# Kernel optimization log

Measured on AMD Instinct MI355X. Metric: run time of the kernel, lower is better.

Reference implementation:

```python
import jax, jax.numpy as jnp
import numpy as np

FOV_UP = 3.0 * np.pi / 180.0
FOV_DOWN = -25.0 * np.pi / 180.0
BIG = 1e9  # penalty to exclude invalid points from nearest-neighbor search


def rv_to_points(rv):
    """Spherical back-projection of a range image [H,W] -> xyz [H,W,3]."""
    H, W = rv.shape
    fov = FOV_UP - FOV_DOWN
    pitch = (1.0 - (jnp.arange(H, dtype=rv.dtype) + 0.5) / H) * fov + FOV_DOWN  # [H]
    yaw = -((jnp.arange(W, dtype=rv.dtype) + 0.5) / W * 2.0 - 1.0) * jnp.pi     # [W]
    cp = jnp.cos(pitch)[:, None]
    sp = jnp.sin(pitch)[:, None]
    x = rv * cp * jnp.cos(yaw)[None, :]
    y = rv * cp * jnp.sin(yaw)[None, :]
    z = rv * sp
    return jnp.stack([x, y, z], axis=-1)


def masked_chamfer(po, mo, pt, mt):
    """Symmetric chamfer (squared distances) between masked point sets.
    po [N,3], mo [N] in {0,1}; pt [M,3], mt [M] in {0,1}."""
    # squared pairwise distances [N,M] without materializing [N,M,3]
    d = (jnp.sum(po * po, axis=-1)[:, None]
         + jnp.sum(pt * pt, axis=-1)[None, :]
         - 2.0 * po @ pt.T)
    d1 = jnp.min(d + BIG * (1.0 - mt)[None, :], axis=1)  # NN dist for each output pt
    d2 = jnp.min(d + BIG * (1.0 - mo)[:, None], axis=0)  # NN dist for each target pt
    m1 = jnp.sum(d1 * mo) / jnp.maximum(jnp.sum(mo), 1.0)
    m2 = jnp.sum(d2 * mt) / jnp.maximum(jnp.sum(mt), 1.0)
    return m1 + m2


def chamfer_forward(rv, target):
    B, S, H, W = rv.shape

    def one(args):
        rv_bs, tgt_bs = args  # [H,W], [4,H,W]
        po = rv_to_points(rv_bs).reshape(-1, 3)
        mo = (rv_bs > 0.0).astype(rv_bs.dtype).reshape(-1)
        pt = jnp.transpose(tgt_bs[1:4], (1, 2, 0)).reshape(-1, 3)
        mt = (tgt_bs[0] > 0.0).astype(rv_bs.dtype).reshape(-1)
        return masked_chamfer(po, mo, pt, mt)

    # sequential over the B*S pairs: only one [N,N] distance matrix live at a time
    per_pair = jax.lax.map(one, (rv.reshape(B * S, H, W),
                                 target.reshape(B * S, 4, H, W)))
    return per_pair.reshape(B, S).T  # [S, B], matches chamfer_distances_tensor[s, b]


def setup_inputs():
    key = jax.random.key(0)
    k1, k2, k3 = jax.random.split(key, 3)
    B, S, H, W = 2, 4, 64, 128
    rv = jax.random.normal(k1, (B, S, H, W), dtype=jnp.float32)
    target = jax.random.normal(k2, (B, S, 4, H, W), dtype=jnp.float32)
    mos_label = jax.random.randint(k3, (B, S, H, W), 0, 2, dtype=jnp.int32)
    return {"rv": rv, "target": target, "mos_label": mos_label, "n_samples": -1}


def reference(rv, target, mos_label, n_samples):
    # n_samples == -1 -> full (non-subsampled) chamfer distance.
    # mos_label is extracted in the original but never affects the returned values.
    tensor = chamfer_forward(rv, target)          # [S, B]
    per_step = jnp.mean(tensor, axis=1)           # chamfer_distances[s] = batch mean
    return per_step, tensor
```

## Files before the change

kernel.cpp:

```cpp
#include <hip/hip_runtime.h>
#include <math.h>

constexpr int kH = 64, kW = 128, kB = 2, kS = 4;
constexpr int kNP = kH * kW;
constexpr int kPairs = kB * kS;
constexpr int kDirs = kPairs * 2;
constexpr float kPen = 32768.0f;
constexpr float kPi = 3.14159265358979323846f;
constexpr float kFovUp = 3.0f * kPi / 180.0f;
constexpr float kFovDown = -25.0f * kPi / 180.0f;

typedef short short8 __attribute__((ext_vector_type(8)));
typedef unsigned short ushort8 __attribute__((ext_vector_type(8)));
typedef float floatx16 __attribute__((ext_vector_type(16)));

constexpr int NCC = 8;
constexpr int CCH = kNP / NCC;
constexpr int NQB = 8;
constexpr int BPD = NQB * NCC;
constexpr int QT = 4;
constexpr int BT = 512;

constexpr size_t OFF_MIN = 524288;
constexpr size_t OFF_MVAL = 655360;
constexpr size_t OFF_DCNT = 655376;
constexpr size_t OFF_ACNT = 655392;

__device__ __forceinline__ unsigned short f2bf(float v) {
  unsigned u = __float_as_uint(v);
  unsigned r = u + 0x7FFFu + ((u >> 16) & 1u);
  return (unsigned short)(r >> 16);
}
__device__ __forceinline__ float bf2f(unsigned short b) {
  return __uint_as_float(((unsigned)b) << 16);
}


__global__ __launch_bounds__(256) void prep_kernel(
    const float* __restrict__ rv, const float* __restrict__ tgt,
    float4* __restrict__ pts, unsigned* __restrict__ minarr,
    float* __restrict__ mval, unsigned* __restrict__ dcnt,
    unsigned* __restrict__ acnt) {
  int idx = blockIdx.x * 256 + threadIdx.x;
  int p = idx >> 13;
  int k = idx & (kNP - 1);
  int h = k >> 7;
  int w = k & 127;

  float r = rv[idx];
  float pitch = (1.0f - (h + 0.5f) * (1.0f / kH)) * (kFovUp - kFovDown) + kFovDown;
  float yaw = -(((w + 0.5f) * (1.0f / kW)) * 2.0f - 1.0f) * kPi;
  float cp = __cosf(pitch), sp = __sinf(pitch);
  float cy = __cosf(yaw), sy = __sinf(yaw);
  float px = r * cp * cy, py = r * cp * sy, pz = r * sp;
  float mo = (r > 0.0f) ? 1.0f : 0.0f;

  const float* tb = tgt + (size_t)p * 4 * kNP;
  float mt = (tb[k] > 0.0f) ? 1.0f : 0.0f;
  float tx = tb[kNP + k], ty = tb[2 * kNP + k], tz = tb[3 * kNP + k];

  float no = px * px + py * py + pz * pz;
  float nt = tx * tx + ty * ty + tz * tz;
  float co = no + kPen * (1.0f - mo);
  float ct = nt + kPen * (1.0f - mt);

  int d0 = 2 * p, d1 = d0 + 1;
  pts[(size_t)d0 * kNP + k] = make_float4(px, py, pz, co);
  pts[(size_t)d1 * kNP + k] = make_float4(tx, ty, tz, ct);

  minarr[(size_t)d0 * kNP + k] = 0xFFFFFFFFu;
  minarr[(size_t)d1 * kNP + k] = 0xFFFFFFFFu;
  if (idx < kDirs) { dcnt[idx] = 0u; mval[idx] = 0.0f; }
  if (idx == kDirs) *acnt = 0u;
}

__global__ __launch_bounds__(BT) void nn_kernel(
    const float4* __restrict__ pts, unsigned* __restrict__ minarr,
    float* __restrict__ mval, unsigned* __restrict__ dcnt,
    unsigned* __restrict__ acnt, float* __restrict__ out) {
  __shared__ __align__(16) unsigned short sc[CCH * 16 + 512];
  __shared__ unsigned s_ticket;
  __shared__ float sw[8], sm[8];

  int bid = blockIdx.x;
  int d = bid >> 6;
  int qb = (bid >> 3) & 7;
  int ch = bid & 7;
  int t = threadIdx.x;

  const float4* cand = pts + (size_t)(d ^ 1) * kNP + ch * CCH;
#pragma unroll
  for (int i = 0; i < 2; ++i) {
    int j = t + i * BT;
    float4 P = cand[j];
    float X = -2.0f * P.x, Y = -2.0f * P.y, Z = -2.0f * P.z;
    float ct = P.w;
    unsigned short Xh = f2bf(X), Yh = f2bf(Y), Zh = f2bf(Z);
    unsigned short Xl = f2bf(X - bf2f(Xh));
    unsigned short Yl = f2bf(Y - bf2f(Yh));
    unsigned short Zl = f2bf(Z - bf2f(Zh));
    unsigned short Ch = f2bf(ct);
    float c1 = ct - bf2f(Ch);
    unsigned short Cl = f2bf(c1);
    unsigned short Cl2 = f2bf(c1 - bf2f(Cl));
    unsigned short* dst = sc + (j >> 5) * 512 + (j & 31) * 8;
    *(ushort8*)dst = (ushort8){Xh, Xl, Xh, Yh, Yl, Yh, Zh, Zl};
    *(ushort8*)(dst + 256) = (ushort8){Zh, Ch, Cl, Cl2, 0, 0, 0, 0};
  }
  __syncthreads();

  int wave = t >> 6, lane = t & 63;
  int col = lane & 31, half = lane >> 5;
  int qbase = d * kNP + qb * 1024 + wave * 128;

  const short one_bf = (short)0x3F80;
  short8 bq[QT];
  float mn[QT];
#pragma unroll
  for (int qt = 0; qt < QT; ++qt) {
    float4 P = pts[qbase + qt * 32 + col];
    unsigned short xh = f2bf(P.x), yh = f2bf(P.y), zh = f2bf(P.z);
    unsigned short xl = f2bf(P.x - bf2f(xh));
    unsigned short yl = f2bf(P.y - bf2f(yh));
    unsigned short zl = f2bf(P.z - bf2f(zh));
    short8 b;
    if (half == 0)
      b = (short8){(short)xh, (short)xh, (short)xl, (short)yh,
                   (short)yh, (short)yl, (short)zh, (short)zh};
    else
      b = (short8){(short)zl, one_bf, one_bf, one_bf, 0, 0, 0, 0};
    bq[qt] = b;
    mn[qt] = 3.0e38f;
  }

  floatx16 zc = {0.0f, 0.0f, 0.0f, 0.0f, 0.0f, 0.0f, 0.0f, 0.0f,
                 0.0f, 0.0f, 0.0f, 0.0f, 0.0f, 0.0f, 0.0f, 0.0f};

  const short8* ap = (const short8*)sc + lane;
  short8 a = ap[0];
#pragma unroll 2
  for (int ctile = 0; ctile < CCH / 32; ++ctile) {
    short8 an = ap[(ctile + 1) * 64];
#pragma unroll
    for (int qt = 0; qt < QT; ++qt) {
      floatx16 dr =
          __builtin_amdgcn_mfma_f32_32x32x16_bf16(a, bq[qt], zc, 0, 0, 0);
      float f0 = fminf(fminf(dr[0], dr[1]), dr[2]);
      float f1 = fminf(fminf(dr[3], dr[4]), dr[5]);
      float f2 = fminf(fminf(dr[6], dr[7]), dr[8]);
      float f3 = fminf(fminf(dr[9], dr[10]), dr[11]);
      float f4 = fminf(fminf(dr[12], dr[13]), dr[14]);
      float g0 = fminf(fminf(f0, f1), dr[15]);
      float g1 = fminf(fminf(f2, f3), f4);
      mn[qt] = fminf(fminf(g0, g1), mn[qt]);
    }
    a = an;
  }

#pragma unroll
  for (int qt = 0; qt < QT; ++qt) {
    float m = fminf(mn[qt], __shfl_xor(mn[qt], 32));
    if (lane < 32) {
      unsigned bb = __float_as_uint(m);
      unsigned e = (bb & 0x80000000u) ? ~bb : (bb | 0x80000000u);
      atomicMin(&minarr[qbase + qt * 32 + lane], e);
    }
  }

  __syncthreads();
  if (t == 0)
    s_ticket = __hip_atomic_fetch_add(&dcnt[d], 1u, __ATOMIC_RELAXED,
                                      __HIP_MEMORY_SCOPE_AGENT);
  __syncthreads();
  if (s_ticket != (unsigned)(BPD - 1)) return;

  float wsum = 0.0f, msum = 0.0f;
#pragma unroll 4
  for (int j = 0; j < kNP / BT; ++j) {
    int k = j * BT + t;
    unsigned u = __hip_atomic_load(&minarr[(size_t)d * kNP + k],
                                   __ATOMIC_RELAXED, __HIP_MEMORY_SCOPE_AGENT);
    unsigned bb = (u & 0x80000000u) ? (u ^ 0x80000000u) : ~u;
    float mnv = __uint_as_float(bb);
    float4 P = pts[(size_t)d * kNP + k];
    if (P.w < 16384.0f) {
      wsum += P.w + mnv;
      msum += 1.0f;
    }
  }
#pragma unroll
  for (int off = 32; off; off >>= 1) {
    wsum += __shfl_down(wsum, off);
    msum += __shfl_down(msum, off);
  }
  if ((t & 63) == 0) { sw[t >> 6] = wsum; sm[t >> 6] = msum; }
  __syncthreads();
  if (t == 0) {
    float ws_ = 0.0f, ms_ = 0.0f;
#pragma unroll
    for (int w2 = 0; w2 < 8; ++w2) { ws_ += sw[w2]; ms_ += sm[w2]; }
    __hip_atomic_store(&mval[d], ws_ / fmaxf(ms_, 1.0f), __ATOMIC_RELAXED,
                       __HIP_MEMORY_SCOPE_AGENT);
    s_ticket = __hip_atomic_fetch_add(acnt, 1u, __ATOMIC_ACQ_REL,
                                      __HIP_MEMORY_SCOPE_AGENT);
  }
  __syncthreads();
  if (s_ticket != (unsigned)(kDirs - 1)) return;
  if (t == 0) {
    float mv[kDirs];
    for (int dd = 0; dd < kDirs; ++dd)
      mv[dd] = __hip_atomic_load(&mval[dd], __ATOMIC_RELAXED,
                                 __HIP_MEMORY_SCOPE_AGENT);
    for (int s = 0; s < kS; ++s) {
      float acc = 0.0f;
      for (int b = 0; b < kB; ++b) {
        int p = b * kS + s;
        float tens = mv[2 * p] + mv[2 * p + 1];
        out[kS + s * kB + b] = tens;
        acc += tens;
      }
      out[s] = acc * (1.0f / kB);
    }
  }
}

extern "C" void kernel_launch(void* const* d_in, const int* in_sizes, int n_in,
                              void* d_out, int out_size, void* d_ws, size_t ws_size,
                              hipStream_t stream) {
  const float* rv = (const float*)d_in[0];
  const float* tgt = (const float*)d_in[1];
  float* ws = (float*)d_ws;
  float4* pts = (float4*)ws;
  unsigned* minarr = (unsigned*)(ws + OFF_MIN);
  float* mval = ws + OFF_MVAL;
  unsigned* dcnt = (unsigned*)(ws + OFF_DCNT);
  unsigned* acnt = (unsigned*)(ws + OFF_ACNT);
  float* out = (float*)d_out;

  hipLaunchKernelGGL(prep_kernel, dim3(kPairs * kNP / 256), dim3(256), 0, stream,
                     rv, tgt, pts, minarr, mval, dcnt, acnt);
  hipLaunchKernelGGL(nn_kernel, dim3(kDirs * NQB * NCC), dim3(BT), 0, stream,
                     pts, minarr, mval, dcnt, acnt, out);
}
```

Baseline: 100.1 us.

## Replace global atomicMin with per-chunk partial minima and hierarchical tail reduction

Each block now writes its per-query minima to a private per-candidate-chunk slice with plain stores instead of doing atomicMin on a shared array. The last of the NCC chunk blocks for each query group reduces those slices, so tail reductions run in parallel across 64 groups rather than in one block per direction. A second ticket level then combines the per-group partial sums into the per-direction mean. This removes atomic contention and the serial 8192-element tail loop, and prep no longer has to initialise the min array. In exchange it uses a larger workspace and adds reads of eight partial arrays.

```diff
diff --git a/kernel.cpp b/kernel.cpp
--- a/kernel.cpp
+++ b/kernel.cpp
@@ -17,14 +17,15 @@
 constexpr int NCC = 8;
 constexpr int CCH = kNP / NCC;
 constexpr int NQB = 8;
-constexpr int BPD = NQB * NCC;
 constexpr int QT = 4;
 constexpr int BT = 512;
 
-constexpr size_t OFF_MIN = 524288;
-constexpr size_t OFF_MVAL = 655360;
-constexpr size_t OFF_DCNT = 655376;
-constexpr size_t OFF_ACNT = 655392;
+constexpr size_t OFF_MINPART = 524288;
+constexpr size_t OFF_QPART = 1572864;
+constexpr size_t OFF_GCNT = 1573120;
+constexpr size_t OFF_DCNT = 1573248;
+constexpr size_t OFF_MVAL = 1573264;
+constexpr size_t OFF_ACNT = 1573280;
 
 __device__ __forceinline__ unsigned short f2bf(float v) {
   unsigned u = __float_as_uint(v);
@@ -38,7 +39,7 @@
 
 __global__ __launch_bounds__(256) void prep_kernel(
     const float* __restrict__ rv, const float* __restrict__ tgt,
-    float4* __restrict__ pts, unsigned* __restrict__ minarr,
+    float4* __restrict__ pts, unsigned* __restrict__ gcnt,
     float* __restrict__ mval, unsigned* __restrict__ dcnt,
     unsigned* __restrict__ acnt) {
   int idx = blockIdx.x * 256 + threadIdx.x;
@@ -68,14 +69,14 @@
   pts[(size_t)d0 * kNP + k] = make_float4(px, py, pz, co);
   pts[(size_t)d1 * kNP + k] = make_float4(tx, ty, tz, ct);
 
-  minarr[(size_t)d0 * kNP + k] = 0xFFFFFFFFu;
-  minarr[(size_t)d1 * kNP + k] = 0xFFFFFFFFu;
+  if (idx < kDirs * NQB) gcnt[idx] = 0u;
   if (idx < kDirs) { dcnt[idx] = 0u; mval[idx] = 0.0f; }
   if (idx == kDirs) *acnt = 0u;
 }
 
 __global__ __launch_bounds__(BT) void nn_kernel(
-    const float4* __restrict__ pts, unsigned* __restrict__ minarr,
+    const float4* __restrict__ pts, unsigned* __restrict__ minpart,
+    float* __restrict__ qpart, unsigned* __restrict__ gcnt,
     float* __restrict__ mval, unsigned* __restrict__ dcnt,
     unsigned* __restrict__ acnt, float* __restrict__ out) {
   __shared__ __align__(16) unsigned short sc[CCH * 16 + 512];
@@ -160,31 +161,34 @@
 #pragma unroll
   for (int qt = 0; qt < QT; ++qt) {
     float m = fminf(mn[qt], __shfl_xor(mn[qt], 32));
-    if (lane < 32) {
-      unsigned bb = __float_as_uint(m);
-      unsigned e = (bb & 0x80000000u) ? ~bb : (bb | 0x80000000u);
-      atomicMin(&minarr[qbase + qt * 32 + lane], e);
-    }
+    if (lane < 32)
+      __hip_atomic_store(
+          &minpart[(size_t)(d * NCC + ch) * kNP + qb * 1024 + wave * 128 +
+                   qt * 32 + lane],
+          __float_as_uint(m), __ATOMIC_RELAXED, __HIP_MEMORY_SCOPE_AGENT);
   }
 
   __syncthreads();
   if (t == 0)
-    s_ticket = __hip_atomic_fetch_add(&dcnt[d], 1u, __ATOMIC_RELAXED,
+    s_ticket = __hip_atomic_fetch_add(&gcnt[d * NQB + qb], 1u, __ATOMIC_RELAXED,
                                       __HIP_MEMORY_SCOPE_AGENT);
   __syncthreads();
-  if (s_ticket != (unsigned)(BPD - 1)) return;
+  if (s_ticket != (unsigned)(NCC - 1)) return;
 
   float wsum = 0.0f, msum = 0.0f;
-#pragma unroll 4
-  for (int j = 0; j < kNP / BT; ++j) {
-    int k = j * BT + t;
-    unsigned u = __hip_atomic_load(&minarr[(size_t)d * kNP + k],
-                                   __ATOMIC_RELAXED, __HIP_MEMORY_SCOPE_AGENT);
-    unsigned bb = (u & 0x80000000u) ? (u ^ 0x80000000u) : ~u;
-    float mnv = __uint_as_float(bb);
-    float4 P = pts[(size_t)d * kNP + k];
+#pragma unroll
+  for (int r = 0; r < 1024 / BT; ++r) {
+    int q = qb * 1024 + r * BT + t;
+    float mv = 3.0e38f;
+#pragma unroll
+    for (int c = 0; c < NCC; ++c) {
+      unsigned u = __hip_atomic_load(&minpart[(size_t)(d * NCC + c) * kNP + q],
+                                     __ATOMIC_RELAXED, __HIP_MEMORY_SCOPE_AGENT);
+      mv = fminf(mv, __uint_as_float(u));
+    }
+    float4 P = pts[(size_t)d * kNP + q];
     if (P.w < 16384.0f) {
-      wsum += P.w + mnv;
+      wsum += P.w + mv;
       msum += 1.0f;
     }
   }
@@ -199,7 +203,29 @@
     float ws_ = 0.0f, ms_ = 0.0f;
 #pragma unroll
     for (int w2 = 0; w2 < 8; ++w2) { ws_ += sw[w2]; ms_ += sm[w2]; }
-    __hip_atomic_store(&mval[d], ws_ / fmaxf(ms_, 1.0f), __ATOMIC_RELAXED,
+    int g = d * NQB + qb;
+    __hip_atomic_store(&qpart[g * 2], ws_, __ATOMIC_RELAXED,
+                       __HIP_MEMORY_SCOPE_AGENT);
+    __hip_atomic_store(&qpart[g * 2 + 1], ms_, __ATOMIC_RELAXED,
+                       __HIP_MEMORY_SCOPE_AGENT);
+    s_ticket = __hip_atomic_fetch_add(&dcnt[d], 1u, __ATOMIC_ACQ_REL,
+                                      __HIP_MEMORY_SCOPE_AGENT);
+  }
+  __syncthreads();
+  if (s_ticket != (unsigned)(NQB - 1)) return;
+
+  if (t == 0) {
+    float W = 0.0f, M = 0.0f;
+#pragma unroll
+    for (int g = 0; g < NQB; ++g) {
+      W += __uint_as_float(__hip_atomic_load(
+          (unsigned*)&qpart[(d * NQB + g) * 2], __ATOMIC_RELAXED,
+          __HIP_MEMORY_SCOPE_AGENT));
+      M += __uint_as_float(__hip_atomic_load(
+          (unsigned*)&qpart[(d * NQB + g) * 2 + 1], __ATOMIC_RELAXED,
+          __HIP_MEMORY_SCOPE_AGENT));
+    }
+    __hip_atomic_store(&mval[d], W / fmaxf(M, 1.0f), __ATOMIC_RELAXED,
                        __HIP_MEMORY_SCOPE_AGENT);
     s_ticket = __hip_atomic_fetch_add(acnt, 1u, __ATOMIC_ACQ_REL,
                                       __HIP_MEMORY_SCOPE_AGENT);
@@ -231,14 +257,16 @@
   const float* tgt = (const float*)d_in[1];
   float* ws = (float*)d_ws;
   float4* pts = (float4*)ws;
-  unsigned* minarr = (unsigned*)(ws + OFF_MIN);
+  unsigned* minpart = (unsigned*)(ws + OFF_MINPART);
+  float* qpart = ws + OFF_QPART;
+  unsigned* gcnt = (unsigned*)(ws + OFF_GCNT);
+  unsigned* dcnt = (unsigned*)(ws + OFF_DCNT);
   float* mval = ws + OFF_MVAL;
-  unsigned* dcnt = (unsigned*)(ws + OFF_DCNT);
   unsigned* acnt = (unsigned*)(ws + OFF_ACNT);
   float* out = (float*)d_out;
 
   hipLaunchKernelGGL(prep_kernel, dim3(kPairs * kNP / 256), dim3(256), 0, stream,
-                     rv, tgt, pts, minarr, mval, dcnt, acnt);
+                     rv, tgt, pts, gcnt, mval, dcnt, acnt);
   hipLaunchKernelGGL(nn_kernel, dim3(kDirs * NQB * NCC), dim3(BT), 0, stream,
-                     pts, minarr, mval, dcnt, acnt, out);
-}
+                     pts, minpart, qpart, gcnt, mval, dcnt, acnt, out);
+}
```

Result: slower. 103.8 us (+3.7%).
